# Performance work log

Hardware: AMD Instinct MI355X
Metric: run time of the kernel (lower is better)

## Reference

```python
import jax, jax.numpy as jnp
import numpy as np

C = 80          # NUM_CLASSES
D = 8525        # total anchors over FPN levels (640 input: 80^2+40^2+20^2+10^2+5^2)
B = 64
EPS = 1e-6


def setup_inputs() -> dict:
    key = jax.random.key(0)
    ks = jax.random.split(key, 8)
    outs = jax.random.normal(ks[0], (B, D, C + 5), dtype=jnp.float32)
    grids = jax.random.uniform(ks[1], (D, 2), dtype=jnp.float32) * 640.0  # anchor centers (px)
    # --- build gres = [gcls(C), centerness(1), g_ltrb(4), mask_pp(1), mask_pos(1), pad(1)] ---
    labels = jax.random.randint(ks[2], (B, D), 0, C)
    mask_pos = (jax.random.uniform(ks[3], (B, D)) < 0.10).astype(jnp.float32)  # in-box positives
    mask_pp = (jax.random.uniform(ks[4], (B, D)) < 0.05).astype(jnp.float32)   # center-radius positives
    gcls = jax.nn.one_hot(labels, C, dtype=jnp.float32) * mask_pos[..., None]
    gcenterness = jax.random.uniform(ks[5], (B, D), dtype=jnp.float32)
    off = jax.random.uniform(ks[6], (B, D, 4), dtype=jnp.float32) * 64.0 + 1.0
    gx = grids[None, :, 0]
    gy = grids[None, :, 1]
    g_ltrb = jnp.stack([gx - off[..., 0], gy - off[..., 1],
                        gx + off[..., 2], gy + off[..., 3]], axis=-1)
    gres = jnp.concatenate([gcls,
                            gcenterness[..., None],
                            g_ltrb,
                            mask_pp[..., None],
                            mask_pos[..., None],
                            jnp.zeros((B, D, 1), jnp.float32)], axis=-1)  # [B, D, 88]
    nums_pos = jax.random.randint(ks[7], (B,), 1, 21).astype(jnp.int32)
    return {"outs": outs, "gres": gres, "grids": grids, "nums_pos": nums_pos}


def _giou(p, g):
    # elementwise GIoU on ltrb boxes, p/g: [..., 4]
    ix1 = jnp.maximum(p[..., 0], g[..., 0]); iy1 = jnp.maximum(p[..., 1], g[..., 1])
    ix2 = jnp.minimum(p[..., 2], g[..., 2]); iy2 = jnp.minimum(p[..., 3], g[..., 3])
    inter = jnp.clip(ix2 - ix1, 0.0) * jnp.clip(iy2 - iy1, 0.0)
    area_p = jnp.clip(p[..., 2] - p[..., 0], 0.0) * jnp.clip(p[..., 3] - p[..., 1], 0.0)
    area_g = jnp.clip(g[..., 2] - g[..., 0], 0.0) * jnp.clip(g[..., 3] - g[..., 1], 0.0)
    union = area_p + area_g - inter
    iou = inter / (union + EPS)
    cx1 = jnp.minimum(p[..., 0], g[..., 0]); cy1 = jnp.minimum(p[..., 1], g[..., 1])
    cx2 = jnp.maximum(p[..., 2], g[..., 2]); cy2 = jnp.maximum(p[..., 3], g[..., 3])
    c_area = (cx2 - cx1) * (cy2 - cy1)
    return iou - (c_area - union) / (c_area + EPS)


def reference(outs, gres, grids, nums_pos):
    np_f = nums_pos.astype(jnp.float32)
    # ---- cls: focal loss over all anchors ----
    pcls = jax.nn.sigmoid(outs[..., :C])          # [B, D, C]
    gcls = gres[..., :C]
    pos_m = (gcls == 1.0).astype(pcls.dtype)
    l_pos = -0.25 * (1.0 - pcls) ** 2 * jnp.log(pcls + EPS) * pos_m
    l_neg = -0.75 * pcls ** 2 * jnp.log(1.0 - pcls + EPS) * (1.0 - pos_m)
    l_cls_pos = jnp.mean(jnp.sum(l_pos, axis=(1, 2)) / np_f)
    l_cls_neg = jnp.mean(jnp.sum(l_neg, axis=(1, 2)) / np_f)
    # ---- conf: BCE(pconf, 1) over center-radius positives ----
    mask_pp = (gres[..., C + 5] == 1.0).astype(outs.dtype)
    pconf = jax.nn.sigmoid(outs[..., C])
    bce = -jnp.log(pconf + EPS)                    # target = ones
    l_conf = 5.0 * jnp.mean(jnp.sum(bce * mask_pp, axis=-1) / np_f)
    # ---- reg: masked GIoU over in-box positives ----
    mask_pos = (gres[..., C + 6] == 1.0).astype(outs.dtype)
    poff = outs[..., C + 1:C + 5]
    gxy = grids[None]                              # [1, D, 2]
    pboxes = jnp.concatenate([gxy - poff[..., :2], gxy + poff[..., 2:]], axis=-1)
    g_ltrb = gres[..., C + 1:C + 5]
    giou = _giou(pboxes, g_ltrb)                   # [B, D]
    gcenter = gres[..., C]
    n_pos = jnp.maximum(jnp.sum(mask_pos), 1.0)
    l_reg = 5.0 * jnp.sum((1.0 - giou) * gcenter * mask_pos) / n_pos
    return l_cls_pos + l_cls_neg + l_conf + l_reg
```

## Files before the change

kernel.cpp:

```cpp
#include <hip/hip_runtime.h>

namespace {

constexpr int   kC    = 80;
constexpr int   kD    = 8525;
constexpr int   kB    = 64;
constexpr float kEps  = 1e-6f;
constexpr int   kOC   = 85;
constexpr int   kGC   = 88;
constexpr int   kBlk  = 256;
constexpr int   kPB   = kD * kOC;
constexpr int   kSpb  = 32;
constexpr int   kRPS  = (kD + kSpb - 1) / kSpb;
constexpr int   kNT   = kB * kSpb;
constexpr int   kQCap = 96;
constexpr int   kQW   = 9;

constexpr float kLog2e = 1.44269504f;
constexpr float kLn2   = 0.69314718f;

__device__ __forceinline__ float wave_reduce(float v) {
#pragma unroll
  for (int o = 32; o > 0; o >>= 1) v += __shfl_down(v, o, 64);
  return v;
}

__device__ __forceinline__ float fast_rcp(float x) {
  return __builtin_amdgcn_rcpf(x);
}

__device__ __forceinline__ float lneg2(float x) {
  const float t = __builtin_amdgcn_exp2f(x * -kLog2e);
  const float p = fast_rcp(1.0f + t);
  return p * p * __builtin_amdgcn_logf(1.000001f - p);
}

__device__ __forceinline__ float lneg2_4(const float4 v) {
  return (lneg2(v.x) + lneg2(v.y)) + (lneg2(v.z) + lneg2(v.w));
}

__global__ __launch_bounds__(kBlk, 8) void floss_fused(
    const float* __restrict__ outs, const float* __restrict__ gres,
    const float* __restrict__ grids, const int* __restrict__ nums_pos,
    float* __restrict__ partials) {
  const int bid = blockIdx.x;
  const int tid = threadIdx.x;
  const int b   = bid >> 5;
  const int sb  = bid & 31;
  const int r0  = sb * kRPS;
  const int r1  = (r0 + kRPS < kD) ? r0 + kRPS : kD;
  const int nrows = r1 - r0;
  const float scale = fast_rcp(64.0f * (float)nums_pos[b]);

  __shared__ float s_q[kQCap * kQW];
  __shared__ int   s_cnt;
  __shared__ float sm[3][kBlk / 64];
  if (tid == 0) s_cnt = 0;

  float accS = 0.f;
  float accT = 0.f;
  float pmO  = 0.f;
  float pr = 0.f, pn = 0.f;

  auto streamPhase = [&]() {
    const int gA = b * kPB + r0 * kOC;
    const int gB = b * kPB + r1 * kOC;
    const int gv = (gA + 3) & ~3;
    const int nvec = (gB - gv) >> 2;
    const int gvend = gv + (nvec << 2);
    float a0 = 0.f, a1 = 0.f, a2 = 0.f, a3 = 0.f;
    if (tid < gv - gA)    a0 += lneg2(outs[gA + tid]);
    if (tid < gB - gvend) a1 += lneg2(outs[gvend + tid]);
    const float4* pv = (const float4*)(outs + gv);
    int v = tid;
    for (; v + 3 * kBlk < nvec; v += 4 * kBlk) {
      const float4 xa = pv[v];
      const float4 xb = pv[v + kBlk];
      const float4 xc = pv[v + 2 * kBlk];
      const float4 xd = pv[v + 3 * kBlk];
      a0 += lneg2_4(xa);
      a1 += lneg2_4(xb);
      a2 += lneg2_4(xc);
      a3 += lneg2_4(xd);
    }
    for (; v < nvec; v += kBlk) a0 += lneg2_4(pv[v]);
    accS += (a0 + a1) + (a2 + a3);
  };

  auto rowStage1 = [&]() {
    for (int rl = tid; rl < nrows; rl += kBlk) {
      const int r   = r0 + rl;
      const int row = b * kD + r;
      const float4 xt  = *(const float4*)(outs + (size_t)row * kOC + 80);
      const float  x84 = outs[(size_t)row * kOC + 84];
      const float4 t1  = *(const float4*)(gres + (size_t)row * kGC + 84);
      accT += ((lneg2(xt.x) + lneg2(xt.y)) +
               (lneg2(xt.z) + lneg2(xt.w))) + lneg2(x84);
      if (t1.y == 1.0f) {
        const float pc = fast_rcp(1.0f + __expf(-xt.x));
        pmO += -5.0f * __logf(pc + kEps) * scale;
      }
      if (t1.z == 1.0f) {
        pn += 1.0f;
        const int slot = atomicAdd(&s_cnt, 1);
        if (slot < kQCap) {
          float* q = s_q + slot * kQW;
          const float2 gxy = *(const float2*)(grids + 2 * r);
          q[0] = __int_as_float(row);
          q[1] = xt.y; q[2] = xt.z; q[3] = xt.w; q[4] = x84;
          q[5] = gxy.x; q[6] = gxy.y;
          q[7] = t1.x;
        }
      }
    }
  };

  auto rowStage2 = [&]() {
    const int nq = (s_cnt < kQCap) ? s_cnt : kQCap;
    const int hh = tid >> 5;
    const int h  = tid & 31;
    for (int e = hh; e < nq; e += 8) {
      const float* q = s_q + e * kQW;
      const int row = __float_as_int(q[0]);
      int cand = -1;
      float4 v = make_float4(0.f, 0.f, 0.f, 0.f);
      if (h < 20) {
        v = *(const float4*)(gres + (size_t)row * kGC + 4 * h);
        if (v.x == 1.0f) cand = 4 * h;
        if (v.y == 1.0f) cand = 4 * h + 1;
        if (v.z == 1.0f) cand = 4 * h + 2;
        if (v.w == 1.0f) cand = 4 * h + 3;
      } else if (h == 20) {
        v = *(const float4*)(gres + (size_t)row * kGC + 80);
      }
#pragma unroll
      for (int m = 16; m > 0; m >>= 1) {
        const int o = __shfl_xor(cand, m, 32);
        cand = (o > cand) ? o : cand;
      }
      if (h == 20 && cand >= 0) {
        const float x  = outs[(size_t)row * kOC + cand];
        const float p  = fast_rcp(1.0f + __expf(-x));
        const float om = 1.0f - p;
        const float lp = -0.25f * om * om * __logf(p + kEps);
        const float ln = -0.75f * p * p * __logf(om + kEps);
        pmO += (lp - ln) * scale;
        const float gx = q[5], gy = q[6];
        const float p0 = gx - q[1], p1 = gy - q[2];
        const float p2 = gx + q[3], p3 = gy + q[4];
        const float g0 = v.y, g1 = v.z, g2 = v.w, g3 = q[7];
        const float iw = fmaxf(fminf(p2, g2) - fmaxf(p0, g0), 0.f);
        const float ih = fmaxf(fminf(p3, g3) - fmaxf(p1, g1), 0.f);
        const float inter = iw * ih;
        const float ap = fmaxf(p2 - p0, 0.f) * fmaxf(p3 - p1, 0.f);
        const float ag = fmaxf(g2 - g0, 0.f) * fmaxf(g3 - g1, 0.f);
        const float un = ap + ag - inter;
        const float iou = inter * fast_rcp(un + kEps);
        const float ca = (fmaxf(p2, g2) - fminf(p0, g0)) *
                         (fmaxf(p3, g3) - fminf(p1, g1));
        const float giou = iou - (ca - un) * fast_rcp(ca + kEps);
        pr += (1.0f - giou) * v.x;
      }
    }
  };

  if (((bid >> 8) ^ bid) & 1) {
    streamPhase();
    __syncthreads();
    rowStage1();
    __syncthreads();
    rowStage2();
  } else {
    __syncthreads();
    rowStage1();
    __syncthreads();
    rowStage2();
    streamPhase();
  }

  float pm = 0.75f * kLn2 * scale * (accT - accS) + pmO;

  const float vm = wave_reduce(pm);
  const float vr = wave_reduce(pr);
  const float vn = wave_reduce(pn);
  const int lane = tid & 63;
  const int w    = tid >> 6;
  if (lane == 0) { sm[0][w] = vm; sm[1][w] = vr; sm[2][w] = vn; }
  __syncthreads();
  if (tid == 0) {
    float m = 0.f, r = 0.f, n = 0.f;
#pragma unroll
    for (int j = 0; j < kBlk / 64; ++j) { m += sm[0][j]; r += sm[1][j]; n += sm[2][j]; }
    partials[bid * 3 + 0] = m;
    partials[bid * 3 + 1] = r;
    partials[bid * 3 + 2] = n;
  }
}

__global__ __launch_bounds__(kBlk) void floss_final(
    const float* __restrict__ partials, float* __restrict__ out) {
  float m = 0.f, r = 0.f, n = 0.f;
  for (int i = threadIdx.x; i < kNT; i += kBlk) {
    m += partials[i * 3 + 0];
    r += partials[i * 3 + 1];
    n += partials[i * 3 + 2];
  }
  __shared__ float sm[3][kBlk / 64];
  m = wave_reduce(m); r = wave_reduce(r); n = wave_reduce(n);
  const int lane = threadIdx.x & 63;
  const int w    = threadIdx.x >> 6;
  if (lane == 0) { sm[0][w] = m; sm[1][w] = r; sm[2][w] = n; }
  __syncthreads();
  if (threadIdx.x == 0) {
    float tm = 0.f, tr = 0.f, tn = 0.f;
#pragma unroll
    for (int j = 0; j < kBlk / 64; ++j) { tm += sm[0][j]; tr += sm[1][j]; tn += sm[2][j]; }
    out[0] = tm + 5.0f * tr / fmaxf(tn, 1.0f);
  }
}

}

extern "C" void kernel_launch(void* const* d_in, const int* in_sizes, int n_in,
                              void* d_out, int out_size, void* d_ws, size_t ws_size,
                              hipStream_t stream) {
  const float* outs     = (const float*)d_in[0];
  const float* gres     = (const float*)d_in[1];
  const float* grids    = (const float*)d_in[2];
  const int*   nums_pos = (const int*)d_in[3];
  float* partials = (float*)d_ws;

  floss_fused<<<kNT, kBlk, 0, stream>>>(outs, gres, grids, nums_pos, partials);
  floss_final<<<1, kBlk, 0, stream>>>(partials, (float*)d_out);
}
```

Measured before the change: 64.39 us.

## Split fused loss kernel into separate row-gather and streaming kernels

The single fused kernel, which alternated the streaming negative-focal pass and the sparse row stages per block, is split into two kernels: one for the per-row conf/reg/gather work and one for the dense streaming reduction over all logits. The streaming kernel also unrolls its main loop to eight float4 loads per iteration. The final reduction now merges two partial arrays. This trades the in-kernel interleaving of latency-bound and bandwidth-bound phases for an extra launch and a second pass over the rows, but lets each kernel keep a simpler register footprint and more loads in flight.

```diff
diff --git a/kernel.cpp b/kernel.cpp
--- a/kernel.cpp
+++ b/kernel.cpp
@@ -39,10 +39,78 @@
   return (lneg2(v.x) + lneg2(v.y)) + (lneg2(v.z) + lneg2(v.w));
 }
 
-__global__ __launch_bounds__(kBlk, 8) void floss_fused(
+__global__ __launch_bounds__(kBlk, 8) void floss_stream(
+    const float* __restrict__ outs, const int* __restrict__ nums_pos,
+    float* __restrict__ part_s) {
+  const int bid = blockIdx.x;
+  const int tid = threadIdx.x;
+  const int b   = bid >> 5;
+  const int sb  = bid & 31;
+  const int r0  = sb * kRPS;
+  const int r1  = (r0 + kRPS < kD) ? r0 + kRPS : kD;
+  const float scale = fast_rcp(64.0f * (float)nums_pos[b]);
+
+  const int gA = b * kPB + r0 * kOC;
+  const int gB = b * kPB + r1 * kOC;
+  const int gv = (gA + 3) & ~3;
+  const int nvec = (gB - gv) >> 2;
+  const int gvend = gv + (nvec << 2);
+
+  float a0 = 0.f, a1 = 0.f, a2 = 0.f, a3 = 0.f,
+        a4 = 0.f, a5 = 0.f, a6 = 0.f, a7 = 0.f;
+  if (tid < gv - gA)    a0 += lneg2(outs[gA + tid]);
+  if (tid < gB - gvend) a1 += lneg2(outs[gvend + tid]);
+  const float4* pv = (const float4*)(outs + gv);
+  int v = tid;
+  for (; v + 7 * kBlk < nvec; v += 8 * kBlk) {
+    const float4 xa = pv[v];
+    const float4 xb = pv[v + kBlk];
+    const float4 xc = pv[v + 2 * kBlk];
+    const float4 xd = pv[v + 3 * kBlk];
+    const float4 xe = pv[v + 4 * kBlk];
+    const float4 xf = pv[v + 5 * kBlk];
+    const float4 xg = pv[v + 6 * kBlk];
+    const float4 xh = pv[v + 7 * kBlk];
+    a0 += lneg2_4(xa);
+    a1 += lneg2_4(xb);
+    a2 += lneg2_4(xc);
+    a3 += lneg2_4(xd);
+    a4 += lneg2_4(xe);
+    a5 += lneg2_4(xf);
+    a6 += lneg2_4(xg);
+    a7 += lneg2_4(xh);
+  }
+  for (; v + 3 * kBlk < nvec; v += 4 * kBlk) {
+    const float4 xa = pv[v];
+    const float4 xb = pv[v + kBlk];
+    const float4 xc = pv[v + 2 * kBlk];
+    const float4 xd = pv[v + 3 * kBlk];
+    a0 += lneg2_4(xa);
+    a1 += lneg2_4(xb);
+    a2 += lneg2_4(xc);
+    a3 += lneg2_4(xd);
+  }
+  for (; v < nvec; v += kBlk) a0 += lneg2_4(pv[v]);
+
+  const float acc = ((a0 + a1) + (a2 + a3)) + ((a4 + a5) + (a6 + a7));
+  const float pm = -0.75f * kLn2 * scale * acc;
+
+  __shared__ float sm[kBlk / 64];
+  const float vm = wave_reduce(pm);
+  if ((tid & 63) == 0) sm[tid >> 6] = vm;
+  __syncthreads();
+  if (tid == 0) {
+    float m = 0.f;
+#pragma unroll
+    for (int j = 0; j < kBlk / 64; ++j) m += sm[j];
+    part_s[bid] = m;
+  }
+}
+
+__global__ __launch_bounds__(kBlk, 8) void floss_rows(
     const float* __restrict__ outs, const float* __restrict__ gres,
     const float* __restrict__ grids, const int* __restrict__ nums_pos,
-    float* __restrict__ partials) {
+    float* __restrict__ part_r) {
   const int bid = blockIdx.x;
   const int tid = threadIdx.x;
   const int b   = bid >> 5;
@@ -56,66 +124,38 @@
   __shared__ int   s_cnt;
   __shared__ float sm[3][kBlk / 64];
   if (tid == 0) s_cnt = 0;
-
-  float accS = 0.f;
-  float accT = 0.f;
-  float pmO  = 0.f;
-  float pr = 0.f, pn = 0.f;
-
-  auto streamPhase = [&]() {
-    const int gA = b * kPB + r0 * kOC;
-    const int gB = b * kPB + r1 * kOC;
-    const int gv = (gA + 3) & ~3;
-    const int nvec = (gB - gv) >> 2;
-    const int gvend = gv + (nvec << 2);
-    float a0 = 0.f, a1 = 0.f, a2 = 0.f, a3 = 0.f;
-    if (tid < gv - gA)    a0 += lneg2(outs[gA + tid]);
-    if (tid < gB - gvend) a1 += lneg2(outs[gvend + tid]);
-    const float4* pv = (const float4*)(outs + gv);
-    int v = tid;
-    for (; v + 3 * kBlk < nvec; v += 4 * kBlk) {
-      const float4 xa = pv[v];
-      const float4 xb = pv[v + kBlk];
-      const float4 xc = pv[v + 2 * kBlk];
-      const float4 xd = pv[v + 3 * kBlk];
-      a0 += lneg2_4(xa);
-      a1 += lneg2_4(xb);
-      a2 += lneg2_4(xc);
-      a3 += lneg2_4(xd);
+  __syncthreads();
+
+  float accT = 0.f, pmO = 0.f, pr = 0.f, pn = 0.f;
+
+  for (int rl = tid; rl < nrows; rl += kBlk) {
+    const int r   = r0 + rl;
+    const int row = b * kD + r;
+    const float4 xt  = *(const float4*)(outs + (size_t)row * kOC + 80);
+    const float  x84 = outs[(size_t)row * kOC + 84];
+    const float4 t1  = *(const float4*)(gres + (size_t)row * kGC + 84);
+    accT += ((lneg2(xt.x) + lneg2(xt.y)) +
+             (lneg2(xt.z) + lneg2(xt.w))) + lneg2(x84);
+    if (t1.y == 1.0f) {
+      const float pc = fast_rcp(1.0f + __expf(-xt.x));
+      pmO += -5.0f * __logf(pc + kEps) * scale;
     }
-    for (; v < nvec; v += kBlk) a0 += lneg2_4(pv[v]);
-    accS += (a0 + a1) + (a2 + a3);
-  };
-
-  auto rowStage1 = [&]() {
-    for (int rl = tid; rl < nrows; rl += kBlk) {
-      const int r   = r0 + rl;
-      const int row = b * kD + r;
-      const float4 xt  = *(const float4*)(outs + (size_t)row * kOC + 80);
-      const float  x84 = outs[(size_t)row * kOC + 84];
-      const float4 t1  = *(const float4*)(gres + (size_t)row * kGC + 84);
-      accT += ((lneg2(xt.x) + lneg2(xt.y)) +
-               (lneg2(xt.z) + lneg2(xt.w))) + lneg2(x84);
-      if (t1.y == 1.0f) {
-        const float pc = fast_rcp(1.0f + __expf(-xt.x));
-        pmO += -5.0f * __logf(pc + kEps) * scale;
-      }
-      if (t1.z == 1.0f) {
-        pn += 1.0f;
-        const int slot = atomicAdd(&s_cnt, 1);
-        if (slot < kQCap) {
-          float* q = s_q + slot * kQW;
-          const float2 gxy = *(const float2*)(grids + 2 * r);
-          q[0] = __int_as_float(row);
-          q[1] = xt.y; q[2] = xt.z; q[3] = xt.w; q[4] = x84;
-          q[5] = gxy.x; q[6] = gxy.y;
-          q[7] = t1.x;
-        }
+    if (t1.z == 1.0f) {
+      pn += 1.0f;
+      const int slot = atomicAdd(&s_cnt, 1);
+      if (slot < kQCap) {
+        float* q = s_q + slot * kQW;
+        const float2 gxy = *(const float2*)(grids + 2 * r);
+        q[0] = __int_as_float(row);
+        q[1] = xt.y; q[2] = xt.z; q[3] = xt.w; q[4] = x84;
+        q[5] = gxy.x; q[6] = gxy.y;
+        q[7] = t1.x;
       }
     }
-  };
-
-  auto rowStage2 = [&]() {
+  }
+  __syncthreads();
+
+  {
     const int nq = (s_cnt < kQCap) ? s_cnt : kQCap;
     const int hh = tid >> 5;
     const int h  = tid & 31;
@@ -162,23 +202,9 @@
         pr += (1.0f - giou) * v.x;
       }
     }
-  };
-
-  if (((bid >> 8) ^ bid) & 1) {
-    streamPhase();
-    __syncthreads();
-    rowStage1();
-    __syncthreads();
-    rowStage2();
-  } else {
-    __syncthreads();
-    rowStage1();
-    __syncthreads();
-    rowStage2();
-    streamPhase();
-  }
-
-  float pm = 0.75f * kLn2 * scale * (accT - accS) + pmO;
+  }
+
+  const float pm = 0.75f * kLn2 * scale * accT + pmO;
 
   const float vm = wave_reduce(pm);
   const float vr = wave_reduce(pr);
@@ -191,19 +217,20 @@
     float m = 0.f, r = 0.f, n = 0.f;
 #pragma unroll
     for (int j = 0; j < kBlk / 64; ++j) { m += sm[0][j]; r += sm[1][j]; n += sm[2][j]; }
-    partials[bid * 3 + 0] = m;
-    partials[bid * 3 + 1] = r;
-    partials[bid * 3 + 2] = n;
+    part_r[bid * 3 + 0] = m;
+    part_r[bid * 3 + 1] = r;
+    part_r[bid * 3 + 2] = n;
   }
 }
 
 __global__ __launch_bounds__(kBlk) void floss_final(
-    const float* __restrict__ partials, float* __restrict__ out) {
+    const float* __restrict__ part_s, const float* __restrict__ part_r,
+    float* __restrict__ out) {
   float m = 0.f, r = 0.f, n = 0.f;
   for (int i = threadIdx.x; i < kNT; i += kBlk) {
-    m += partials[i * 3 + 0];
-    r += partials[i * 3 + 1];
-    n += partials[i * 3 + 2];
+    m += part_s[i] + part_r[i * 3 + 0];
+    r += part_r[i * 3 + 1];
+    n += part_r[i * 3 + 2];
   }
   __shared__ float sm[3][kBlk / 64];
   m = wave_reduce(m); r = wave_reduce(r); n = wave_reduce(n);
@@ -228,8 +255,10 @@
   const float* gres     = (const float*)d_in[1];
   const float* grids    = (const float*)d_in[2];
   const int*   nums_pos = (const int*)d_in[3];
-  float* partials = (float*)d_ws;
-
-  floss_fused<<<kNT, kBlk, 0, stream>>>(outs, gres, grids, nums_pos, partials);
-  floss_final<<<1, kBlk, 0, stream>>>(partials, (float*)d_out);
-}
+  float* part_s = (float*)d_ws;
+  float* part_r = (float*)d_ws + kNT;
+
+  floss_rows<<<kNT, kBlk, 0, stream>>>(outs, gres, grids, nums_pos, part_r);
+  floss_stream<<<kNT, kBlk, 0, stream>>>(outs, nums_pos, part_s);
+  floss_final<<<1, kBlk, 0, stream>>>(part_s, part_r, (float*)d_out);
+}
```

Result: slower. 70.53 us (+9.5%).

## Halve block count and software-pipeline streaming loads with double-buffered registers

Applied to the files above, without the earlier changes.

Cuts the number of slices per batch from 32 to 16, so each block covers twice as many rows, doubles the positive queue capacity, and relaxes launch bounds to allow more registers per thread. The streaming loop now keeps two banks of eight float4 loads in registers and issues the next bank before computing the current one, aiming for more memory-level parallelism per wave. The cost is higher register pressure, lower occupancy, fewer blocks to spread across CUs, and a coarser phase-ordering toggle.

```diff
diff --git a/kernel.cpp b/kernel.cpp
--- a/kernel.cpp
+++ b/kernel.cpp
@@ -2,7 +2,6 @@
 
 namespace {
 
-constexpr int   kC    = 80;
 constexpr int   kD    = 8525;
 constexpr int   kB    = 64;
 constexpr float kEps  = 1e-6f;
@@ -10,10 +9,10 @@
 constexpr int   kGC   = 88;
 constexpr int   kBlk  = 256;
 constexpr int   kPB   = kD * kOC;
-constexpr int   kSpb  = 32;
+constexpr int   kSpb  = 16;
 constexpr int   kRPS  = (kD + kSpb - 1) / kSpb;
 constexpr int   kNT   = kB * kSpb;
-constexpr int   kQCap = 96;
+constexpr int   kQCap = 192;
 constexpr int   kQW   = 9;
 
 constexpr float kLog2e = 1.44269504f;
@@ -39,14 +38,14 @@
   return (lneg2(v.x) + lneg2(v.y)) + (lneg2(v.z) + lneg2(v.w));
 }
 
-__global__ __launch_bounds__(kBlk, 8) void floss_fused(
+__global__ __launch_bounds__(kBlk, 4) void floss_fused(
     const float* __restrict__ outs, const float* __restrict__ gres,
     const float* __restrict__ grids, const int* __restrict__ nums_pos,
     float* __restrict__ partials) {
   const int bid = blockIdx.x;
   const int tid = threadIdx.x;
-  const int b   = bid >> 5;
-  const int sb  = bid & 31;
+  const int b   = bid >> 4;
+  const int sb  = bid & 15;
   const int r0  = sb * kRPS;
   const int r1  = (r0 + kRPS < kD) ? r0 + kRPS : kD;
   const int nrows = r1 - r0;
@@ -68,23 +67,52 @@
     const int gv = (gA + 3) & ~3;
     const int nvec = (gB - gv) >> 2;
     const int gvend = gv + (nvec << 2);
-    float a0 = 0.f, a1 = 0.f, a2 = 0.f, a3 = 0.f;
+    float a0 = 0.f, a1 = 0.f, a2 = 0.f, a3 = 0.f,
+          a4 = 0.f, a5 = 0.f, a6 = 0.f, a7 = 0.f;
     if (tid < gv - gA)    a0 += lneg2(outs[gA + tid]);
     if (tid < gB - gvend) a1 += lneg2(outs[gvend + tid]);
     const float4* pv = (const float4*)(outs + gv);
-    int v = tid;
+
+    float4 A[8], Bq[8];
+    auto load8 = [&](float4* dst, int roundBase) {
+#pragma unroll
+      for (int j = 0; j < 8; ++j) dst[j] = pv[roundBase + tid + j * kBlk];
+    };
+    auto comp8 = [&](const float4* src) {
+      a0 += lneg2_4(src[0]); a1 += lneg2_4(src[1]);
+      a2 += lneg2_4(src[2]); a3 += lneg2_4(src[3]);
+      a4 += lneg2_4(src[4]); a5 += lneg2_4(src[5]);
+      a6 += lneg2_4(src[6]); a7 += lneg2_4(src[7]);
+    };
+
+    const int nfull = nvec / (8 * kBlk);
+    if (nfull > 0) {
+      load8(A, 0);
+      int r = 0;
+      while (r + 2 <= nfull) {
+        load8(Bq, (r + 1) * 8 * kBlk);
+        comp8(A);
+        if (r + 2 < nfull) {
+          load8(A, (r + 2) * 8 * kBlk);
+          comp8(Bq);
+        } else {
+          comp8(Bq);
+        }
+        r += 2;
+      }
+      if (r < nfull) comp8(A);
+    }
+    int v = nfull * 8 * kBlk + tid;
     for (; v + 3 * kBlk < nvec; v += 4 * kBlk) {
       const float4 xa = pv[v];
       const float4 xb = pv[v + kBlk];
       const float4 xc = pv[v + 2 * kBlk];
       const float4 xd = pv[v + 3 * kBlk];
-      a0 += lneg2_4(xa);
-      a1 += lneg2_4(xb);
-      a2 += lneg2_4(xc);
-      a3 += lneg2_4(xd);
+      a0 += lneg2_4(xa); a1 += lneg2_4(xb);
+      a2 += lneg2_4(xc); a3 += lneg2_4(xd);
     }
     for (; v < nvec; v += kBlk) a0 += lneg2_4(pv[v]);
-    accS += (a0 + a1) + (a2 + a3);
+    accS += ((a0 + a1) + (a2 + a3)) + ((a4 + a5) + (a6 + a7));
   };
 
   auto rowStage1 = [&]() {
@@ -164,7 +192,7 @@
     }
   };
 
-  if (((bid >> 8) ^ bid) & 1) {
+  if (bid & 1) {
     streamPhase();
     __syncthreads();
     rowStage1();
@@ -178,7 +206,7 @@
     streamPhase();
   }
 
-  float pm = 0.75f * kLn2 * scale * (accT - accS) + pmO;
+  const float pm = 0.75f * kLn2 * scale * (accT - accS) + pmO;
 
   const float vm = wave_reduce(pm);
   const float vr = wave_reduce(pr);
```

After: 65.83 us. +2.3%, slower.
